# Performance work log

Measured on AMD Instinct MI355X. Metric: run time of the kernel, lower is better.

The kernel has to match this reference:

```python
import jax, jax.numpy as jnp
import numpy as np

B, T, C = 4, 2048, 2048
H, HS = 16, 128  # num_heads, head_size; H*HS == C


def setup_inputs() -> dict:
    key = jax.random.key(0)
    k1, k2, k3, k4 = jax.random.split(key, 4)
    x = jax.random.normal(k1, (B, T, C), dtype=jnp.float32)
    # nn.Linear weights are [out, in]; scale ~ kaiming-uniform-ish
    w_qkv = jax.random.normal(k2, (3 * C, C), dtype=jnp.float32) * (1.0 / np.sqrt(C))
    w_proj = jax.random.normal(k3, (C, C), dtype=jnp.float32) * (1.0 / np.sqrt(C))
    b_proj = jax.random.normal(k4, (C,), dtype=jnp.float32) * 0.01
    return {"x": x, "w_qkv": w_qkv, "w_proj": w_proj, "b_proj": b_proj}


def reference(x, w_qkv, w_proj, b_proj):
    Bq, Tq, Cq = x.shape
    qkv = jnp.einsum("btc,dc->btd", x, w_qkv)  # [B,T,3C]
    q, k, v = jnp.split(qkv, 3, axis=2)
    # [B,T,C] -> [B,H,T,hs]
    q = q.reshape(Bq, Tq, H, HS).transpose(0, 2, 1, 3)
    k = k.reshape(Bq, Tq, H, HS).transpose(0, 2, 1, 3)
    v = v.reshape(Bq, Tq, H, HS).transpose(0, 2, 1, 3)
    scale = 1.0 / np.sqrt(HS)
    scores = jnp.einsum("bhqd,bhkd->bhqk", q, k) * scale  # [B,H,T,T]
    causal = jnp.tril(jnp.ones((Tq, Tq), dtype=bool))
    scores = jnp.where(causal, scores, jnp.finfo(scores.dtype).min)
    attn = jax.nn.softmax(scores, axis=-1)
    out = jnp.einsum("bhqk,bhkd->bhqd", attn, v)  # [B,H,T,hs]
    out = out.transpose(0, 2, 1, 3).reshape(Bq, Tq, Cq)
    out = jnp.einsum("btc,dc->btd", out, w_proj) + b_proj
    return out
```

## Files before the change

kernel.cpp:

```cpp
#include <hip/hip_runtime.h>

#define Tq 2048
#define Cq 2048
#define Hn 16
#define HSz 128
#define Bq 4
#define SCALE_QK 0.08838834764831845f

typedef __bf16 bf16x8 __attribute__((ext_vector_type(8)));
typedef float f32x4 __attribute__((ext_vector_type(4)));
typedef unsigned short u16;
typedef u16 u16x4 __attribute__((ext_vector_type(4)));

__device__ __forceinline__ u16 f2bf(float f) {
  unsigned u = __builtin_bit_cast(unsigned, f);
  u += 0x7FFFu + ((u >> 16) & 1u);
  return (u16)(u >> 16);
}

__device__ __forceinline__ bf16x8 ld_frag(const void* p) {
  bf16x8 v; __builtin_memcpy(&v, p, 16); return v;
}

__device__ __forceinline__ void glds16(void* lds, const void* g) {
  __builtin_amdgcn_global_load_lds(
      (const __attribute__((address_space(1))) void*)g,
      (__attribute__((address_space(3))) void*)lds, 16, 0, 0);
}

__global__ void cvt_bf16(const float* __restrict__ in, u16* __restrict__ out, int n) {
  int i = (blockIdx.x * 256 + threadIdx.x) * 4;
  if (i >= n) return;
  f32x4 v; __builtin_memcpy(&v, in + i, 16);
  u16x4 o;
  o[0] = f2bf(v[0]); o[1] = f2bf(v[1]); o[2] = f2bf(v[2]); o[3] = f2bf(v[3]);
  __builtin_memcpy(out + i, &o, 8);
}


#define LDFRAGS(slotB, AF, BF) do { \
  const char* sb_ = LdsB + (size_t)(slotB) * 49152; \
  _Pragma("unroll") for (int mi_ = 0; mi_ < 4; ++mi_) \
  _Pragma("unroll") for (int kk_ = 0; kk_ < 2; ++kk_) { \
    const int row_ = wm*64 + mi_*16 + lr; \
    AF[mi_*2+kk_] = ld_frag(sb_ + row_*128 + ((kk_*64 + lg*16) ^ swz)); } \
  _Pragma("unroll") for (int nf_ = 0; nf_ < 4; ++nf_) \
  _Pragma("unroll") for (int kk_ = 0; kk_ < 2; ++kk_) { \
    const int row_ = wn*64 + nf_*16 + lr; \
    BF[nf_*2+kk_] = ld_frag(sb_ + 32768 + row_*128 + ((kk_*64 + lg*16) ^ swz)); } \
  } while(0)

#define STAGEK(t2, slotB) do { \
    const int k0_ = (t2) * 64; \
    u16* ab_ = Lds + (size_t)(slotB) * 24576; \
    _Pragma("unroll") for (int i_ = 0; i_ < 4; ++i_) { \
      const int c_ = w*4 + i_; \
      glds16(ab_ + c_*512, A + (size_t)(m0 + c_*8 + (l >> 3)) * K + k0_ + srcE); } \
    _Pragma("unroll") for (int i_ = 0; i_ < 2; ++i_) { \
      const int c_ = w*2 + i_; \
      glds16(ab_ + 16384 + c_*512, Bm + (size_t)(n0 + c_*8 + (l >> 3)) * K + k0_ + srcE); } \
  } while(0)

#define MFMA32(AF, BF) do { \
    __builtin_amdgcn_s_setprio(1); \
    _Pragma("unroll") for (int mi_ = 0; mi_ < 4; ++mi_) \
    _Pragma("unroll") for (int nf_ = 0; nf_ < 4; ++nf_) \
    _Pragma("unroll") for (int kk_ = 0; kk_ < 2; ++kk_) \
      acc[mi_][nf_] = __builtin_amdgcn_mfma_f32_16x16x32_bf16( \
          AF[mi_*2+kk_], BF[nf_*2+kk_], acc[mi_][nf_], 0, 0, 0); \
    __builtin_amdgcn_s_setprio(0); \
  } while(0)

#define BAR asm volatile("s_barrier" ::: "memory")
#define FENCE(n) asm volatile("s_waitcnt vmcnt(" #n ")" ::: "memory")

#define TILE(t, Ac, Bc, An, Bn, slR, slS) do { \
    FENCE(0); BAR; \
    if ((t) + 1 < NT) LDFRAGS(slR, An, Bn); \
    if ((t) + 2 < NT) STAGEK((t) + 2, slS); \
    MFMA32(Ac, Bc); \
  } while(0)

template <int EPI>
__global__ __launch_bounds__(512, 2)
void gemm256(const u16* __restrict__ A, const u16* __restrict__ Bm, int K,
             u16* __restrict__ qout, u16* __restrict__ kout, u16* __restrict__ vtout,
             float* __restrict__ fout, const float* __restrict__ bias) {
  __shared__ u16 Lds3[3 * 24576];
  const int tid = threadIdx.x;
  const int w = tid >> 6, l = tid & 63;
  const int wm = w >> 1, wn = w & 1;
  const int lr = l & 15, lg = l >> 4;
  const int swz = (lr & 7) << 4;

  const int nwg = gridDim.x * gridDim.y;
  int ow = blockIdx.y * gridDim.x + blockIdx.x;
  ow = (ow & 7) * (nwg >> 3) + (ow >> 3);
  const int bx = ow % gridDim.x, by = ow / gridDim.x;
  const int m0 = by * 256, n0 = bx * 128;

  const int srcE = ((l & 7) ^ (l >> 3)) << 3;

  u16* Lds = Lds3;
  const char* LdsB = (const char*)Lds3;

  f32x4 acc[4][4];
  const f32x4 fz = {0.f, 0.f, 0.f, 0.f};
#pragma unroll
  for (int i = 0; i < 4; ++i)
#pragma unroll
    for (int j = 0; j < 4; ++j) acc[i][j] = fz;

  bf16x8 afE[8], afO[8], bfE[8], bfO[8];
  const int NT = K >> 6;

  STAGEK(0, 0);
  STAGEK(1, 1);
  FENCE(6);
  BAR;
  LDFRAGS(0, afE, bfE);

  int r_ = 1, s_ = 2;
#pragma unroll 1
  for (int t = 0; t < NT; t += 2) {
    TILE(t, afE, bfE, afO, bfO, r_, s_);
    { int ns = (s_ == 2) ? 0 : s_ + 1; r_ = s_; s_ = ns; }
    TILE(t + 1, afO, bfO, afE, bfE, r_, s_);
    { int ns = (s_ == 2) ? 0 : s_ + 1; r_ = s_; s_ = ns; }
  }

  if constexpr (EPI == 0) {
#pragma unroll
    for (int mi = 0; mi < 4; ++mi) {
      const int trow = m0 + wm * 64 + mi * 16 + lg * 4;
      const int bb = trow >> 11, tt0 = trow & 2047;
#pragma unroll
      for (int nf = 0; nf < 4; ++nf) {
        const int d = n0 + wn * 64 + nf * 16 + lr;
        const int part = d >> 11;
        const int dd = d & 2047;
        const int hh = dd >> 7, hs = dd & 127;
        if (part == 2) {
          u16x4 pk;
          pk[0] = f2bf(acc[mi][nf][0]); pk[1] = f2bf(acc[mi][nf][1]);
          pk[2] = f2bf(acc[mi][nf][2]); pk[3] = f2bf(acc[mi][nf][3]);
          size_t off = ((size_t)(bb * Hn + hh) * HSz + hs) * Tq + tt0;
          __builtin_memcpy(&vtout[off], &pk, 8);
        } else {
          u16* dst = (part == 0) ? qout : kout;
#pragma unroll
          for (int rr = 0; rr < 4; ++rr) {
            size_t off = ((size_t)(bb * Hn + hh) * Tq + (tt0 + rr)) * HSz + hs;
            dst[off] = f2bf(acc[mi][nf][rr]);
          }
        }
      }
    }
  } else {
#pragma unroll
    for (int mi = 0; mi < 4; ++mi) {
      const int trow = m0 + wm * 64 + mi * 16 + lg * 4;
#pragma unroll
      for (int nf = 0; nf < 4; ++nf) {
        const int d = n0 + wn * 64 + nf * 16 + lr;
        const float bv = bias[d];
#pragma unroll
        for (int rr = 0; rr < 4; ++rr)
          fout[(size_t)(trow + rr) * Cq + d] = acc[mi][nf][rr] + bv;
      }
    }
  }
}

#define KVB 64
__global__ __launch_bounds__(256, 2)
void attn_fwd(const u16* __restrict__ qb, const u16* __restrict__ kb,
              const u16* __restrict__ vtb, u16* __restrict__ ob) {
  __shared__ u16 Ks[2 * KVB * HSz];
  __shared__ u16 Vs[2 * HSz * KVB];
  __shared__ u16 Ps[4 * 32 * 32];

  const int tid = threadIdx.x;
  const int w = tid >> 6, l = tid & 63;
  const int lr = l & 15, lg = l >> 4;
  const int bh = blockIdx.x, jj0 = blockIdx.y;
  const int b = bh >> 4, h = bh & 15;

  const u16* qp = qb + (size_t)bh * Tq * HSz;
  const u16* kp = kb + (size_t)bh * Tq * HSz;
  const u16* vp = vtb + (size_t)bh * HSz * Tq;

#pragma unroll 1
  for (int pass = 0; pass < 2; ++pass) {
    const int qt = pass ? (15 - jj0) : jj0;
    const int q0 = qt * 128;

    bf16x8 qf[2][4];
#pragma unroll
    for (int mi = 0; mi < 2; ++mi)
#pragma unroll
      for (int kk = 0; kk < 4; ++kk) {
        int row = q0 + w * 32 + mi * 16 + lr;
        qf[mi][kk] = ld_frag(qp + (size_t)row * HSz + kk * 32 + lg * 8);
      }

    const f32x4 fz = {0.f, 0.f, 0.f, 0.f};
    f32x4 o[2][8];
    float mrow[2][4], lrow[2][4];
#pragma unroll
    for (int mi = 0; mi < 2; ++mi) {
#pragma unroll
      for (int nj = 0; nj < 8; ++nj) o[mi][nj] = fz;
#pragma unroll
      for (int rr = 0; rr < 4; ++rr) { mrow[mi][rr] = -1e30f; lrow[mi][rr] = 0.f; }
    }

    const int nt = 2 * (qt + 1);

    auto stage = [&](int t, int buf) {
      const int kv0 = t * KVB;
      u16* Kb = &Ks[buf * (KVB * HSz)];
      u16* Vb = &Vs[buf * (HSz * KVB)];
#pragma unroll
      for (int i = 0; i < 4; ++i) {
        int c = w * 4 + i;
        {
          int r = c * 4 + lg;
          int cb = (lr * 16) ^ ((r & 7) << 4);
          glds16(&Kb[c * 512], (const char*)(kp + (size_t)(kv0 + r) * HSz) + cb);
        }
        {
          int r = c * 8 + (l >> 3);
          int cb = ((l & 7) * 16) ^ ((r & 7) << 4);
          glds16(&Vb[c * 512], (const char*)(vp + (size_t)r * Tq + kv0) + cb);
        }
      }
    };

    stage(0, 0);
#pragma unroll 1
    for (int t = 0; t < nt; ++t) {
      const int buf = t & 1;
      if (t + 1 < nt) {
        stage(t + 1, buf ^ 1);
        asm volatile("s_waitcnt vmcnt(8)\ns_barrier" ::: "memory");
      } else {
        asm volatile("s_waitcnt vmcnt(0)\ns_barrier" ::: "memory");
      }
      const u16* Ksb = &Ks[buf * (KVB * HSz)];
      const u16* Vsb = &Vs[buf * (HSz * KVB)];
      const int kv0 = t * KVB;

      f32x4 s[2][4];
#pragma unroll
      for (int mi = 0; mi < 2; ++mi)
#pragma unroll
        for (int nj = 0; nj < 4; ++nj) s[mi][nj] = fz;
#pragma unroll
      for (int kk = 0; kk < 4; ++kk) {
        bf16x8 kf[4];
#pragma unroll
        for (int nj = 0; nj < 4; ++nj) {
          int row = nj * 16 + lr;
          int cb = (kk * 64 + lg * 16) ^ ((row & 7) << 4);
          kf[nj] = ld_frag((const char*)Ksb + row * 256 + cb);
        }
        __builtin_amdgcn_s_setprio(1);
#pragma unroll
        for (int mi = 0; mi < 2; ++mi)
#pragma unroll
          for (int nj = 0; nj < 4; ++nj)
            s[mi][nj] = __builtin_amdgcn_mfma_f32_16x16x32_bf16(qf[mi][kk], kf[nj], s[mi][nj], 0, 0, 0);
        __builtin_amdgcn_s_setprio(0);
      }

      const bool diag = (t >= nt - 2);
      float corr[2][4];
      bool grew = false;
#pragma unroll
      for (int mi = 0; mi < 2; ++mi) {
#pragma unroll
        for (int rr = 0; rr < 4; ++rr) {
          const int qrow = q0 + w * 32 + mi * 16 + lg * 4 + rr;
          float pm = -1e30f;
#pragma unroll
          for (int nj = 0; nj < 4; ++nj) {
            float v = s[mi][nj][rr] * SCALE_QK;
            if (diag && (kv0 + nj * 16 + lr) > qrow) v = -1e30f;
            s[mi][nj][rr] = v;
            pm = fmaxf(pm, v);
          }
          pm = fmaxf(pm, __shfl_xor(pm, 1));
          pm = fmaxf(pm, __shfl_xor(pm, 2));
          pm = fmaxf(pm, __shfl_xor(pm, 4));
          pm = fmaxf(pm, __shfl_xor(pm, 8));
          float mo = mrow[mi][rr];
          float mn = fmaxf(mo, pm);
          corr[mi][rr] = __expf(mo - mn);
          grew |= (pm > mo);
          mrow[mi][rr] = mn;
          float rs = 0.f;
#pragma unroll
          for (int nj = 0; nj < 4; ++nj) {
            float p = __expf(s[mi][nj][rr] - mn);
            s[mi][nj][rr] = p;
            rs += p;
          }
          rs += __shfl_xor(rs, 1);
          rs += __shfl_xor(rs, 2);
          rs += __shfl_xor(rs, 4);
          rs += __shfl_xor(rs, 8);
          lrow[mi][rr] = lrow[mi][rr] * corr[mi][rr] + rs;
        }
      }
      if (__any(grew)) {
#pragma unroll
        for (int mi = 0; mi < 2; ++mi)
#pragma unroll
          for (int nj = 0; nj < 8; ++nj)
#pragma unroll
            for (int rr = 0; rr < 4; ++rr) o[mi][nj][rr] *= corr[mi][rr];
      }

      char* pw = (char*)Ps + w * 2048;
#pragma unroll
      for (int kk = 0; kk < 2; ++kk) {
#pragma unroll
        for (int mi = 0; mi < 2; ++mi)
#pragma unroll
          for (int jj = 0; jj < 2; ++jj) {
            int nj = kk * 2 + jj;
#pragma unroll
            for (int rr = 0; rr < 4; ++rr) {
              int prow = mi * 16 + lg * 4 + rr;
              int pcb = (jj * 16 + lr) * 2;
              *(u16*)(pw + ((prow * 64 + pcb) ^ ((prow & 7) << 4))) = f2bf(s[mi][nj][rr]);
            }
          }
        bf16x8 pa[2];
#pragma unroll
        for (int mi = 0; mi < 2; ++mi) {
          int prow = mi * 16 + lr;
          pa[mi] = ld_frag(pw + ((prow * 64 + lg * 16) ^ ((prow & 7) << 4)));
        }
        __builtin_amdgcn_s_setprio(1);
#pragma unroll
        for (int nj = 0; nj < 8; ++nj) {
          int vrow = nj * 16 + lr;
          int cb = (kk * 64 + lg * 16) ^ ((vrow & 7) << 4);
          bf16x8 vf = ld_frag((const char*)Vsb + vrow * 128 + cb);
#pragma unroll
          for (int mi = 0; mi < 2; ++mi)
            o[mi][nj] = __builtin_amdgcn_mfma_f32_16x16x32_bf16(pa[mi], vf, o[mi][nj], 0, 0, 0);
        }
        __builtin_amdgcn_s_setprio(0);
      }

      asm volatile("s_barrier" ::: "memory");
    }

#pragma unroll
    for (int mi = 0; mi < 2; ++mi)
#pragma unroll
      for (int rr = 0; rr < 4; ++rr) {
        int trow = q0 + w * 32 + mi * 16 + lg * 4 + rr;
        float inv = 1.f / lrow[mi][rr];
#pragma unroll
        for (int nj = 0; nj < 8; ++nj) {
          int d = nj * 16 + lr;
          ob[((size_t)b * Tq + trow) * Cq + h * HSz + d] = f2bf(o[mi][nj][rr] * inv);
        }
      }
  }
}

extern "C" void kernel_launch(void* const* d_in, const int* in_sizes, int n_in,
                              void* d_out, int out_size, void* d_ws, size_t ws_size,
                              hipStream_t stream) {
  const float* x = (const float*)d_in[0];
  const float* w_qkv = (const float*)d_in[1];
  const float* w_proj = (const float*)d_in[2];
  const float* b_proj = (const float*)d_in[3];
  float* out = (float*)d_out;

  char* ws = (char*)d_ws;
  u16* xb     = (u16*)(ws);
  u16* wqkvb  = (u16*)(ws + (size_t)33554432);
  u16* wprojb = (u16*)(ws + (size_t)58720256);
  u16* qbp    = (u16*)(ws + (size_t)67108864);
  u16* kbp    = (u16*)(ws + (size_t)100663296);
  u16* vtbp   = (u16*)(ws + (size_t)134217728);
  (void)in_sizes; (void)n_in; (void)out_size; (void)ws_size;

  cvt_bf16<<<16384, 256, 0, stream>>>(x, xb, 16777216);
  cvt_bf16<<<12288, 256, 0, stream>>>(w_qkv, wqkvb, 12582912);
  cvt_bf16<<<4096, 256, 0, stream>>>(w_proj, wprojb, 4194304);

  gemm256<0><<<dim3(48, 32), 512, 0, stream>>>(xb, wqkvb, 2048, qbp, kbp, vtbp, nullptr, nullptr);

  attn_fwd<<<dim3(64, 8), 256, 0, stream>>>(qbp, kbp, vtbp, xb);

  gemm256<1><<<dim3(16, 32), 512, 0, stream>>>(xb, wprojb, 2048, nullptr, nullptr, nullptr, out, b_proj);
}
```

Baseline: 473.7 us.

## Split attention query tile across eight waves of sixteen rows each

```diff
diff --git a/kernel.cpp b/kernel.cpp
--- a/kernel.cpp
+++ b/kernel.cpp
@@ -173,12 +173,12 @@
 }
 
 #define KVB 64
-__global__ __launch_bounds__(256, 2)
+__global__ __launch_bounds__(512, 4)
 void attn_fwd(const u16* __restrict__ qb, const u16* __restrict__ kb,
               const u16* __restrict__ vtb, u16* __restrict__ ob) {
   __shared__ u16 Ks[2 * KVB * HSz];
   __shared__ u16 Vs[2 * HSz * KVB];
-  __shared__ u16 Ps[4 * 32 * 32];
+  __shared__ u16 Ps[8 * 16 * 32];
 
   const int tid = threadIdx.x;
   const int w = tid >> 6, l = tid & 63;
@@ -195,25 +195,20 @@
     const int qt = pass ? (15 - jj0) : jj0;
     const int q0 = qt * 128;
 
-    bf16x8 qf[2][4];
-#pragma unroll
-    for (int mi = 0; mi < 2; ++mi)
-#pragma unroll
-      for (int kk = 0; kk < 4; ++kk) {
-        int row = q0 + w * 32 + mi * 16 + lr;
-        qf[mi][kk] = ld_frag(qp + (size_t)row * HSz + kk * 32 + lg * 8);
-      }
+    bf16x8 qf[4];
+#pragma unroll
+    for (int kk = 0; kk < 4; ++kk) {
+      int row = q0 + w * 16 + lr;
+      qf[kk] = ld_frag(qp + (size_t)row * HSz + kk * 32 + lg * 8);
+    }
 
     const f32x4 fz = {0.f, 0.f, 0.f, 0.f};
-    f32x4 o[2][8];
-    float mrow[2][4], lrow[2][4];
-#pragma unroll
-    for (int mi = 0; mi < 2; ++mi) {
-#pragma unroll
-      for (int nj = 0; nj < 8; ++nj) o[mi][nj] = fz;
-#pragma unroll
-      for (int rr = 0; rr < 4; ++rr) { mrow[mi][rr] = -1e30f; lrow[mi][rr] = 0.f; }
-    }
+    f32x4 o[8];
+    float mrow[4], lrow[4];
+#pragma unroll
+    for (int nj = 0; nj < 8; ++nj) o[nj] = fz;
+#pragma unroll
+    for (int rr = 0; rr < 4; ++rr) { mrow[rr] = -1e30f; lrow[rr] = 0.f; }
 
     const int nt = 2 * (qt + 1);
 
@@ -222,8 +217,8 @@
       u16* Kb = &Ks[buf * (KVB * HSz)];
       u16* Vb = &Vs[buf * (HSz * KVB)];
 #pragma unroll
-      for (int i = 0; i < 4; ++i) {
-        int c = w * 4 + i;
+      for (int i = 0; i < 2; ++i) {
+        int c = w * 2 + i;
         {
           int r = c * 4 + lg;
           int cb = (lr * 16) ^ ((r & 7) << 4);
@@ -243,7 +238,7 @@
       const int buf = t & 1;
       if (t + 1 < nt) {
         stage(t + 1, buf ^ 1);
-        asm volatile("s_waitcnt vmcnt(8)\ns_barrier" ::: "memory");
+        asm volatile("s_waitcnt vmcnt(4)\ns_barrier" ::: "memory");
       } else {
         asm volatile("s_waitcnt vmcnt(0)\ns_barrier" ::: "memory");
       }
@@ -251,11 +246,9 @@
       const u16* Vsb = &Vs[buf * (HSz * KVB)];
       const int kv0 = t * KVB;
 
-      f32x4 s[2][4];
-#pragma unroll
-      for (int mi = 0; mi < 2; ++mi)
-#pragma unroll
-        for (int nj = 0; nj < 4; ++nj) s[mi][nj] = fz;
+      f32x4 s[4];
+#pragma unroll
+      for (int nj = 0; nj < 4; ++nj) s[nj] = fz;
 #pragma unroll
       for (int kk = 0; kk < 4; ++kk) {
         bf16x8 kf[4];
@@ -267,91 +260,75 @@
         }
         __builtin_amdgcn_s_setprio(1);
 #pragma unroll
-        for (int mi = 0; mi < 2; ++mi)
-#pragma unroll
-          for (int nj = 0; nj < 4; ++nj)
-            s[mi][nj] = __builtin_amdgcn_mfma_f32_16x16x32_bf16(qf[mi][kk], kf[nj], s[mi][nj], 0, 0, 0);
+        for (int nj = 0; nj < 4; ++nj)
+          s[nj] = __builtin_amdgcn_mfma_f32_16x16x32_bf16(qf[kk], kf[nj], s[nj], 0, 0, 0);
         __builtin_amdgcn_s_setprio(0);
       }
 
       const bool diag = (t >= nt - 2);
-      float corr[2][4];
+      float corr[4];
       bool grew = false;
 #pragma unroll
-      for (int mi = 0; mi < 2; ++mi) {
-#pragma unroll
-        for (int rr = 0; rr < 4; ++rr) {
-          const int qrow = q0 + w * 32 + mi * 16 + lg * 4 + rr;
-          float pm = -1e30f;
-#pragma unroll
-          for (int nj = 0; nj < 4; ++nj) {
-            float v = s[mi][nj][rr] * SCALE_QK;
-            if (diag && (kv0 + nj * 16 + lr) > qrow) v = -1e30f;
-            s[mi][nj][rr] = v;
-            pm = fmaxf(pm, v);
+      for (int rr = 0; rr < 4; ++rr) {
+        const int qrow = q0 + w * 16 + lg * 4 + rr;
+        float pm = -1e30f;
+#pragma unroll
+        for (int nj = 0; nj < 4; ++nj) {
+          float v = s[nj][rr] * SCALE_QK;
+          if (diag && (kv0 + nj * 16 + lr) > qrow) v = -1e30f;
+          s[nj][rr] = v;
+          pm = fmaxf(pm, v);
+        }
+        pm = fmaxf(pm, __shfl_xor(pm, 1));
+        pm = fmaxf(pm, __shfl_xor(pm, 2));
+        pm = fmaxf(pm, __shfl_xor(pm, 4));
+        pm = fmaxf(pm, __shfl_xor(pm, 8));
+        float mo = mrow[rr];
+        float mn = fmaxf(mo, pm);
+        corr[rr] = __expf(mo - mn);
+        grew |= (pm > mo);
+        mrow[rr] = mn;
+        float rs = 0.f;
+#pragma unroll
+        for (int nj = 0; nj < 4; ++nj) {
+          float p = __expf(s[nj][rr] - mn);
+          s[nj][rr] = p;
+          rs += p;
+        }
+        rs += __shfl_xor(rs, 1);
+        rs += __shfl_xor(rs, 2);
+        rs += __shfl_xor(rs, 4);
+        rs += __shfl_xor(rs, 8);
+        lrow[rr] = lrow[rr] * corr[rr] + rs;
+      }
+      if (__any(grew)) {
+#pragma unroll
+        for (int nj = 0; nj < 8; ++nj)
+#pragma unroll
+          for (int rr = 0; rr < 4; ++rr) o[nj][rr] *= corr[rr];
+      }
+
+      char* pw = (char*)Ps + w * 1024;
+#pragma unroll
+      for (int kk = 0; kk < 2; ++kk) {
+#pragma unroll
+        for (int jj = 0; jj < 2; ++jj) {
+          int nj = kk * 2 + jj;
+#pragma unroll
+          for (int rr = 0; rr < 4; ++rr) {
+            int prow = lg * 4 + rr;
+            int pcb = (jj * 16 + lr) * 2;
+            *(u16*)(pw + ((prow * 64 + pcb) ^ ((prow & 7) << 4))) = f2bf(s[nj][rr]);
           }
-          pm = fmaxf(pm, __shfl_xor(pm, 1));
-          pm = fmaxf(pm, __shfl_xor(pm, 2));
-          pm = fmaxf(pm, __shfl_xor(pm, 4));
-          pm = fmaxf(pm, __shfl_xor(pm, 8));
-          float mo = mrow[mi][rr];
-          float mn = fmaxf(mo, pm);
-          corr[mi][rr] = __expf(mo - mn);
-          grew |= (pm > mo);
-          mrow[mi][rr] = mn;
-          float rs = 0.f;
-#pragma unroll
-          for (int nj = 0; nj < 4; ++nj) {
-            float p = __expf(s[mi][nj][rr] - mn);
-            s[mi][nj][rr] = p;
-            rs += p;
-          }
-          rs += __shfl_xor(rs, 1);
-          rs += __shfl_xor(rs, 2);
-          rs += __shfl_xor(rs, 4);
-          rs += __shfl_xor(rs, 8);
-          lrow[mi][rr] = lrow[mi][rr] * corr[mi][rr] + rs;
-        }
-      }
-      if (__any(grew)) {
-#pragma unroll
-        for (int mi = 0; mi < 2; ++mi)
-#pragma unroll
-          for (int nj = 0; nj < 8; ++nj)
-#pragma unroll
-            for (int rr = 0; rr < 4; ++rr) o[mi][nj][rr] *= corr[mi][rr];
-      }
-
-      char* pw = (char*)Ps + w * 2048;
-#pragma unroll
-      for (int kk = 0; kk < 2; ++kk) {
-#pragma unroll
-        for (int mi = 0; mi < 2; ++mi)
-#pragma unroll
-          for (int jj = 0; jj < 2; ++jj) {
-            int nj = kk * 2 + jj;
-#pragma unroll
-            for (int rr = 0; rr < 4; ++rr) {
-              int prow = mi * 16 + lg * 4 + rr;
-              int pcb = (jj * 16 + lr) * 2;
-              *(u16*)(pw + ((prow * 64 + pcb) ^ ((prow & 7) << 4))) = f2bf(s[mi][nj][rr]);
-            }
-          }
-        bf16x8 pa[2];
-#pragma unroll
-        for (int mi = 0; mi < 2; ++mi) {
-          int prow = mi * 16 + lr;
-          pa[mi] = ld_frag(pw + ((prow * 64 + lg * 16) ^ ((prow & 7) << 4)));
-        }
+        }
+        bf16x8 pa = ld_frag(pw + ((lr * 64 + lg * 16) ^ ((lr & 7) << 4)));
         __builtin_amdgcn_s_setprio(1);
 #pragma unroll
         for (int nj = 0; nj < 8; ++nj) {
           int vrow = nj * 16 + lr;
           int cb = (kk * 64 + lg * 16) ^ ((vrow & 7) << 4);
           bf16x8 vf = ld_frag((const char*)Vsb + vrow * 128 + cb);
-#pragma unroll
-          for (int mi = 0; mi < 2; ++mi)
-            o[mi][nj] = __builtin_amdgcn_mfma_f32_16x16x32_bf16(pa[mi], vf, o[mi][nj], 0, 0, 0);
+          o[nj] = __builtin_amdgcn_mfma_f32_16x16x32_bf16(pa, vf, o[nj], 0, 0, 0);
         }
         __builtin_amdgcn_s_setprio(0);
       }
@@ -360,17 +337,15 @@
     }
 
 #pragma unroll
-    for (int mi = 0; mi < 2; ++mi)
-#pragma unroll
-      for (int rr = 0; rr < 4; ++rr) {
-        int trow = q0 + w * 32 + mi * 16 + lg * 4 + rr;
-        float inv = 1.f / lrow[mi][rr];
-#pragma unroll
-        for (int nj = 0; nj < 8; ++nj) {
-          int d = nj * 16 + lr;
-          ob[((size_t)b * Tq + trow) * Cq + h * HSz + d] = f2bf(o[mi][nj][rr] * inv);
-        }
-      }
+    for (int rr = 0; rr < 4; ++rr) {
+      int trow = q0 + w * 16 + lg * 4 + rr;
+      float inv = 1.f / lrow[rr];
+#pragma unroll
+      for (int nj = 0; nj < 8; ++nj) {
+        int d = nj * 16 + lr;
+        ob[((size_t)b * Tq + trow) * Cq + h * HSz + d] = f2bf(o[nj][rr] * inv);
+      }
+    }
   }
 }
 
@@ -398,7 +373,7 @@
 
   gemm256<0><<<dim3(48, 32), 512, 0, stream>>>(xb, wqkvb, 2048, qbp, kbp, vtbp, nullptr, nullptr);
 
-  attn_fwd<<<dim3(64, 8), 256, 0, stream>>>(qbp, kbp, vtbp, xb);
+  attn_fwd<<<dim3(64, 8), 512, 0, stream>>>(qbp, kbp, vtbp, xb);
 
   gemm256<1><<<dim3(16, 32), 512, 0, stream>>>(xb, wprojb, 2048, nullptr, nullptr, nullptr, out, b_proj);
 }
```

Result: slower. 485.3 us (+2.5%).
